# Optimization experiments

Hardware: AMD Instinct MI355X
Metric: run time of the kernel (lower is better)

The kernel has to match this reference:

```python
import jax, jax.numpy as jnp
import numpy as np

N_EMBD = 1024
N_HEAD = 16
HEAD_DIM = N_EMBD // N_HEAD


def setup_inputs() -> dict:
    key = jax.random.key(0)
    k1, k2, k3, k4, k5 = jax.random.split(key, 5)
    B, T, C = 4, 2048, N_EMBD
    s = 1.0 / np.sqrt(C)
    return {
        "x": jax.random.normal(k1, (B, T, C), dtype=jnp.float32),
        "W_attn": jax.random.normal(k2, (C, 3 * C), dtype=jnp.float32) * s,
        "b_attn": jnp.zeros((3 * C,), dtype=jnp.float32),
        "W_proj": jax.random.normal(k3, (C, C), dtype=jnp.float32) * s,
        "b_proj": jnp.zeros((C,), dtype=jnp.float32),
    }


def reference(x, W_attn, b_attn, W_proj, b_proj):
    B, T, C = x.shape
    H, D = N_HEAD, HEAD_DIM
    # fused QKV projection
    qkv = x @ W_attn + b_attn                       # [B,T,3C]
    q, k, v = jnp.split(qkv, 3, axis=2)
    q = q.reshape(B, T, H, D).transpose(0, 2, 1, 3)  # [B,H,T,D]
    k = k.reshape(B, T, H, D).transpose(0, 2, 1, 3)
    v = v.reshape(B, T, H, D).transpose(0, 2, 1, 3)
    # causal scaled dot-product attention
    scale = 1.0 / jnp.sqrt(jnp.asarray(D, dtype=x.dtype))
    scores = jnp.einsum('bhqd,bhkd->bhqk', q, k) * scale  # [B,H,T,T]
    causal = jnp.tril(jnp.ones((T, T), dtype=bool))
    scores = jnp.where(causal[None, None], scores, jnp.finfo(x.dtype).min)
    attn = jax.nn.softmax(scores, axis=-1)
    y = jnp.einsum('bhqk,bhkd->bhqd', attn, v)      # [B,H,T,D]
    y = y.transpose(0, 2, 1, 3).reshape(B, T, C)
    return y @ W_proj + b_proj
```

## Files before the change

kernel.cpp:

```cpp
#include <hip/hip_runtime.h>
#include <hip/hip_bf16.h>
#include <cstdint>

#define B_ 4
#define T_ 2048
#define C_ 1024
#define H_ 16
#define D_ 64
#define M_ (B_*T_)
#define N3 (3*C_)

typedef __bf16 bf16;
typedef __bf16 bf16x8 __attribute__((ext_vector_type(8)));
typedef __bf16 bf16x4 __attribute__((ext_vector_type(4)));
typedef float  floatx4 __attribute__((ext_vector_type(4)));

__device__ __forceinline__ void gl_lds16(const bf16* g, bf16* l) {
  __builtin_amdgcn_global_load_lds(
      (__attribute__((address_space(1))) void*)(void*)g,
      (__attribute__((address_space(3))) void*)(void*)l,
      16, 0, 0);
}

__device__ __forceinline__ uint32_t pack_bf16_trunc(float lo, float hi) {
  union { float f; uint32_t u; } a, b;
  a.f = lo; b.f = hi;
  return (a.u >> 16) | (b.u & 0xffff0000u);
}

__global__ void cast_to_bf16(const float* __restrict__ in, bf16* __restrict__ out, int n) {
  int i = (blockIdx.x * blockDim.x + threadIdx.x) * 4;
  if (i < n) {
    const float4 f = *(const float4*)(in + i);
    bf16x4 o;
    o.x = (bf16)f.x; o.y = (bf16)f.y; o.z = (bf16)f.z; o.w = (bf16)f.w;
    *(bf16x4*)(out + i) = o;
  }
}

__global__ void transpose_cast(const float* __restrict__ in, bf16* __restrict__ out,
                               int R, int C) {
  __shared__ float tile[32][33];
  int r0 = blockIdx.y * 32, c0 = blockIdx.x * 32;
  int tx = threadIdx.x & 31, ty = threadIdx.x >> 5;
  #pragma unroll
  for (int j = 0; j < 32; j += 8)
    tile[ty + j][tx] = in[(size_t)(r0 + ty + j) * C + c0 + tx];
  __syncthreads();
  #pragma unroll
  for (int j = 0; j < 32; j += 8)
    out[(size_t)(c0 + ty + j) * R + r0 + tx] = (bf16)tile[tx][ty + j];
}

__global__ __launch_bounds__(256)
void transpose_v(const bf16* __restrict__ in, bf16* __restrict__ out) {
  __shared__ __attribute__((aligned(16))) bf16 tileN[64 * 64];
  const int tid = threadIdx.x;
  const int bh = blockIdx.z;
  const int t0 = blockIdx.x * 64;
  const int sk = tid >> 2, scc = tid & 3;
  {
    const bf16* p = in + ((size_t)bh * T_ + t0 + sk) * D_ + scc * 16;
    const bf16x8 r0 = *(const bf16x8*)p;
    const bf16x8 r1 = *(const bf16x8*)(p + 8);
    *(bf16x8*)(tileN + sk * 64 + ((2 * scc)     ^ (sk & 7)) * 8) = r0;
    *(bf16x8*)(tileN + sk * 64 + ((2 * scc + 1) ^ (sk & 7)) * 8) = r1;
  }
  __syncthreads();
  const int tc = (tid & 7) * 8;
  #pragma unroll
  for (int half = 0; half < 2; half++) {
    const int d = (tid >> 3) + half * 32;
    bf16x8 o;
    #pragma unroll
    for (int j = 0; j < 8; j++) {
      const int slot = tc + j;
      const int row = (slot & 3) + 4 * ((slot >> 3) & 3) + 16 * ((slot >> 2) & 1)
                    + 32 * (slot >> 5);
      o[j] = tileN[row * 64 + (((d >> 3) ^ (row & 7)) * 8) + (d & 7)];
    }
    *(bf16x8*)(out + ((size_t)bh * D_ + d) * T_ + t0 + tc) = o;
  }
}

template<int MODE>
__global__ __launch_bounds__(256)
void gemm_bt(const bf16* __restrict__ A, const bf16* __restrict__ Bt,
             const float* __restrict__ bias, float* __restrict__ out,
             bf16* __restrict__ qo, bf16* __restrict__ ko, bf16* __restrict__ vo,
             int M, int N, int K)
{
  __shared__ __attribute__((aligned(16))) bf16 As[128 * 32];
  __shared__ __attribute__((aligned(16))) bf16 Bs[128 * 32];

  const int tid  = threadIdx.x;
  const int w    = tid >> 6;
  const int lane = tid & 63;
  const int quad = lane >> 4;
  const int l16  = lane & 15;
  const int wm   = w & 1, wn = w >> 1;
  const int m0   = blockIdx.y * 128, n0 = blockIdx.x * 128;

  floatx4 acc[4][4] = {};

  const int lrow = lane >> 2;
  const int lk   = (lane & 3) * 8;

  const bf16* aptr = A  + (size_t)(m0 + w * 32 + lrow) * K + lk;
  const bf16* bptr = Bt + (size_t)(n0 + w * 32 + lrow) * K + lk;
  bf16* asl = As + w * 1024;
  bf16* bsl = Bs + w * 1024;

  for (int k0 = 0; k0 < K; k0 += 32) {
    gl_lds16(aptr,          asl);
    gl_lds16(aptr + 16 * K, asl + 512);
    gl_lds16(bptr,          bsl);
    gl_lds16(bptr + 16 * K, bsl + 512);
    aptr += 32; bptr += 32;
    __syncthreads();

    bf16x8 af[4], bfb[4];
    #pragma unroll
    for (int i = 0; i < 4; i++)
      af[i] = *(const bf16x8*)(As + (wm * 64 + i * 16 + l16) * 32 + quad * 8);
    #pragma unroll
    for (int i = 0; i < 4; i++)
      bfb[i] = *(const bf16x8*)(Bs + (wn * 64 + i * 16 + l16) * 32 + quad * 8);
    #pragma unroll
    for (int mi = 0; mi < 4; mi++)
      #pragma unroll
      for (int ni = 0; ni < 4; ni++)
        acc[mi][ni] = __builtin_amdgcn_mfma_f32_16x16x32_bf16(af[mi], bfb[ni], acc[mi][ni], 0, 0, 0);
    __syncthreads();
  }

  #pragma unroll
  for (int mi = 0; mi < 4; mi++) {
    #pragma unroll
    for (int ni = 0; ni < 4; ni++) {
      const int col = n0 + wn * 64 + ni * 16 + l16;
      const float bv = bias[col];
      #pragma unroll
      for (int r = 0; r < 4; r++) {
        const int row = m0 + wm * 64 + mi * 16 + quad * 4 + r;
        const float val = acc[mi][ni][r] + bv;
        if (MODE == 0) {
          const int b = row >> 11, t = row & 2047;
          const int s = col >> 10, c = col & 1023;
          const int h = c >> 6,  d = c & 63;
          bf16* dst = (s == 0) ? qo : (s == 1) ? ko : vo;
          dst[((size_t)(b * H_ + h) * T_ + t) * D_ + d] = (bf16)val;
        } else {
          out[(size_t)row * N + col] = val;
        }
      }
    }
  }
}

__device__ __forceinline__ void stage8(const bf16* g, int K, bf16* lds, int lane) {
  const int r = lane >> 3, s = (lane & 7) ^ r;
  gl_lds16(g + (size_t)r * K + s * 8, lds);
}
__device__ __forceinline__ void stage_half(const bf16* g, int K, bf16* lds, int wv, int lane) {
  stage8(g + (size_t)(wv * 16) * K,     K, lds + (wv * 16) * 64, lane);
  stage8(g + (size_t)(wv * 16 + 8) * K, K, lds + (wv * 16 + 8) * 64, lane);
}

#define GBAR  __builtin_amdgcn_s_barrier()
#define WLGKM do { asm volatile("s_waitcnt lgkmcnt(0)"); __builtin_amdgcn_sched_barrier(0); } while (0)
#define WVM4  do { asm volatile("s_waitcnt vmcnt(4)");   __builtin_amdgcn_sched_barrier(0); } while (0)

template<int MODE>
__global__ __launch_bounds__(512, 2)
void gemm256(const bf16* __restrict__ A, const bf16* __restrict__ Bt,
             const float* __restrict__ bias, float* __restrict__ out,
             bf16* __restrict__ qo, bf16* __restrict__ ko, bf16* __restrict__ vo,
             int M, int N, int K)
{
  __shared__ __attribute__((aligned(16))) bf16 As[2][256 * 64];
  __shared__ __attribute__((aligned(16))) bf16 Bs[2][256 * 64];

  const int tid  = threadIdx.x;
  const int wv   = tid >> 6, lane = tid & 63;
  const int quad = lane >> 4, l16 = lane & 15;
  const int wm   = wv >> 2, wn = wv & 3;
  const int NTT  = K >> 6;

  const int nbx = gridDim.x;
  const int nwg = nbx * gridDim.y;
  const int bid = blockIdx.y * nbx + blockIdx.x;
  const int cpx = nwg >> 3;
  const int swz = (bid & 7) * cpx + (bid >> 3);
  const int n0  = (swz % nbx) * 256, m0 = (swz / nbx) * 256;

  floatx4 acc[8][4] = {};

  const bf16* Abase = A  + (size_t)m0 * K;
  const bf16* Bbase = Bt + (size_t)n0 * K;

  stage_half(Abase,                  K, As[0],            wv, lane);
  stage_half(Abase + (size_t)128*K,  K, As[0] + 128 * 64, wv, lane);
  stage_half(Bbase,                  K, Bs[0],            wv, lane);
  stage_half(Bbase + (size_t)128*K,  K, Bs[0] + 128 * 64, wv, lane);
  stage_half(Bbase + 64,             K, Bs[1],            wv, lane);
  stage_half(Abase + 64,             K, As[1],            wv, lane);
  WVM4;
  GBAR;

#define LOADA(qm)                                                          \
  _Pragma("unroll")                                                        \
  for (int mi = 0; mi < 4; mi++) {                                         \
    const int row = wm * 128 + (qm) * 64 + mi * 16 + l16;                  \
    const bf16* rp = bufA + row * 64;                                      \
    af[mi][0] = *(const bf16x8*)(rp + (( quad      ^ (row & 7)) * 8));     \
    af[mi][1] = *(const bf16x8*)(rp + (((4 | quad) ^ (row & 7)) * 8));     \
  }
#define LOADB(qn)                                                          \
  _Pragma("unroll")                                                        \
  for (int ni = 0; ni < 2; ni++) {                                         \
    const int row = wn * 64 + (qn) * 32 + ni * 16 + l16;                   \
    const bf16* rp = bufB + row * 64;                                      \
    bfr[(qn)*2+ni][0] = *(const bf16x8*)(rp + (( quad      ^ (row & 7)) * 8)); \
    bfr[(qn)*2+ni][1] = *(const bf16x8*)(rp + (((4 | quad) ^ (row & 7)) * 8)); \
  }
#define MM(qm, qn)                                                         \
  __builtin_amdgcn_s_setprio(1);                                           \
  _Pragma("unroll")                                                        \
  for (int mi = 0; mi < 4; mi++)                                           \
    _Pragma("unroll")                                                      \
    for (int ni = 0; ni < 2; ni++) {                                       \
      acc[(qm)*4+mi][(qn)*2+ni] = __builtin_amdgcn_mfma_f32_16x16x32_bf16( \
          af[mi][0], bfr[(qn)*2+ni][0], acc[(qm)*4+mi][(qn)*2+ni], 0, 0, 0); \
      acc[(qm)*4+mi][(qn)*2+ni] = __builtin_amdgcn_mfma_f32_16x16x32_bf16( \
          af[mi][1], bfr[(qn)*2+ni][1], acc[(qm)*4+mi][(qn)*2+ni], 0, 0, 0); \
    }                                                                      \
  __builtin_amdgcn_s_setprio(0);

  #pragma unroll 1
  for (int t = 0; t < NTT; t++) {
    const int cur = t & 1;
    const bf16* bufA = As[cur];
    const bf16* bufB = Bs[cur];
    bf16* nA = As[cur ^ 1];
    bf16* nB = Bs[cur ^ 1];
    bf16* cA = As[cur];
    bf16* cB = Bs[cur];
    const int kn1 = (t + 1) * 64, kn2 = (t + 2) * 64;
    const bool h1 = (t + 1 < NTT), h2 = (t + 2 < NTT);

    bf16x8 af[4][2], bfr[4][2];

    LOADA(0);
    LOADB(0);
    if (h1) stage_half(Abase + (size_t)128 * K + kn1, K, nA + 128 * 64, wv, lane);
    GBAR;
    WLGKM;
    MM(0, 0);
    GBAR;

    LOADB(1);
    if (h1) stage_half(Bbase + (size_t)128 * K + kn1, K, nB + 128 * 64, wv, lane);
    GBAR;
    WLGKM;
    MM(0, 1);
    GBAR;

    LOADA(1);
    if (h2) stage_half(Bbase + kn2, K, cB, wv, lane);
    GBAR;
    WLGKM;
    MM(1, 0);
    GBAR;

    if (h2) stage_half(Abase + kn2, K, cA, wv, lane);
    GBAR;
    MM(1, 1);
    WVM4;
    GBAR;
  }

#undef LOADA
#undef LOADB
#undef MM

  #pragma unroll
  for (int mi8 = 0; mi8 < 8; mi8++) {
    #pragma unroll
    for (int nf = 0; nf < 4; nf++) {
      const int col = n0 + wn * 64 + nf * 16 + l16;
      const float bv = bias[col];
      #pragma unroll
      for (int r = 0; r < 4; r++) {
        const int row = m0 + wm * 128 + mi8 * 16 + quad * 4 + r;
        const float val = acc[mi8][nf][r] + bv;
        if (MODE == 0) {
          const int b = row >> 11, tt = row & 2047;
          const int s = col >> 10, c = col & 1023;
          const int h = c >> 6, d = c & 63;
          bf16* dst = (s == 0) ? qo : (s == 1) ? ko : vo;
          dst[((size_t)(b * H_ + h) * T_ + tt) * D_ + d] = (bf16)val;
        } else {
          out[(size_t)row * N + col] = val;
        }
      }
    }
  }
}

__global__ __launch_bounds__(256)
void attn_kernel(const bf16* __restrict__ Q, const bf16* __restrict__ Kp,
                 const bf16* __restrict__ Vtp, bf16* __restrict__ Y)
{
  __shared__ __attribute__((aligned(16))) bf16 Ks[2][64 * 72];
  __shared__ __attribute__((aligned(16))) bf16 Vs[2][64 * 72];

  const int tid  = threadIdx.x;
  const int w    = tid >> 6, lane = tid & 63;
  const int quad = lane >> 4, l16 = lane & 15;
  const int bh = blockIdx.x;
  const int b = bh >> 4, h = bh & 15;

  const int sk = tid >> 2;
  const int sc = (tid & 3) * 16;

  const float SC = 0.125f * 1.44269504088896f;

  const int qt = 15 - (int)blockIdx.y;
  const int q0 = qt * 128;
  const int nch = 2 * qt + 2;

  bf16x8 qf[2][2];
  #pragma unroll
  for (int mt = 0; mt < 2; mt++) {
    const bf16* qp = Q + ((size_t)bh * T_ + q0 + mt * 64 + w * 16 + l16) * D_ + quad * 8;
    qf[mt][0] = *(const bf16x8*)qp;
    qf[mt][1] = *(const bf16x8*)(qp + 32);
  }

  floatx4 o[2][4] = {};
  float l_r[2] = {0.f, 0.f};

  const bf16* kpp = Kp  + (size_t)bh * T_ * D_ + (size_t)sk * D_ + sc;
  const bf16* vpp = Vtp + (size_t)bh * D_ * T_ + (size_t)sk * T_ + sc;

  {
    const bf16x8 k0 = *(const bf16x8*)kpp, k1 = *(const bf16x8*)(kpp + 8);
    const bf16x8 v0 = *(const bf16x8*)vpp, v1 = *(const bf16x8*)(vpp + 8);
    bf16* kd = Ks[0] + sk * 72 + sc;
    *(bf16x8*)kd = k0; *(bf16x8*)(kd + 8) = k1;
    bf16* vd = Vs[0] + sk * 72 + sc;
    *(bf16x8*)vd = v0; *(bf16x8*)(vd + 8) = v1;
    kpp += 64 * D_; vpp += 64;
  }
  __syncthreads();

  #pragma unroll 1
  for (int c = 0; c < nch; c++) {
    const int cur = c & 1;

    bf16x8 nk0, nk1, nv0, nv1;
    const bool have = (c + 1 < nch);
    if (have) {
      nk0 = *(const bf16x8*)kpp; nk1 = *(const bf16x8*)(kpp + 8);
      nv0 = *(const bf16x8*)vpp; nv1 = *(const bf16x8*)(vpp + 8);
      kpp += 64 * D_; vpp += 64;
    }

    const bf16* KsC = Ks[cur];
    const bf16* VsC = Vs[cur];
    const int kv0 = c * 64;
    const bool act0 = (c < nch - 1);

    floatx4 s[2][4];
    #pragma unroll
    for (int nt = 0; nt < 4; nt++) {
      const bf16x8 kf0 = *(const bf16x8*)(KsC + (nt * 16 + l16) * 72 + quad * 8);
      const bf16x8 kf1 = *(const bf16x8*)(KsC + (nt * 16 + l16) * 72 + 32 + quad * 8);
      if (act0) {
        floatx4 z = {};
        z = __builtin_amdgcn_mfma_f32_16x16x32_bf16(kf0, qf[0][0], z, 0, 0, 0);
        s[0][nt] = __builtin_amdgcn_mfma_f32_16x16x32_bf16(kf1, qf[0][1], z, 0, 0, 0);
      }
      floatx4 z = {};
      z = __builtin_amdgcn_mfma_f32_16x16x32_bf16(kf0, qf[1][0], z, 0, 0, 0);
      s[1][nt] = __builtin_amdgcn_mfma_f32_16x16x32_bf16(kf1, qf[1][1], z, 0, 0, 0);
    }

    bf16x8 vfr[4][2];
    #pragma unroll
    for (int nt = 0; nt < 4; nt++) {
      vfr[nt][0] = *(const bf16x8*)(VsC + (nt * 16 + l16) * 72 + quad * 8);
      vfr[nt][1] = *(const bf16x8*)(VsC + (nt * 16 + l16) * 72 + 32 + quad * 8);
    }

    #pragma unroll
    for (int mt = 0; mt < 2; mt++) {
      if (mt == 0 && !act0) continue;
      const bool diag = (c == 2 * qt + mt);
      const int qrow = q0 + mt * 64 + w * 16 + l16;
      float e[4][4];
      float ls0 = 0.f, ls1 = 0.f;
      #pragma unroll
      for (int nt = 0; nt < 4; nt++) {
        #pragma unroll
        for (int r = 0; r < 4; r++) {
          float x = s[mt][nt][r];
          if (diag) {
            if (kv0 + nt * 16 + quad * 4 + r > qrow) x = -1e30f;
          }
          const float ev = __builtin_amdgcn_exp2f(fmaf(x, SC, -8.f));
          e[nt][r] = ev;
          if (nt & 1) ls1 += ev; else ls0 += ev;
        }
      }
      l_r[mt] += ls0 + ls1;

      union { uint32_t u[4]; bf16x8 v; } pa0, pa1;
      #pragma unroll
      for (int jj = 0; jj < 4; jj++) {
        pa0.u[jj] = __builtin_amdgcn_perm(
            __float_as_uint(e[(jj >> 1)][(jj & 1) * 2 + 1]),
            __float_as_uint(e[(jj >> 1)][(jj & 1) * 2]), 0x07060302u);
        pa1.u[jj] = __builtin_amdgcn_perm(
            __float_as_uint(e[2 + (jj >> 1)][(jj & 1) * 2 + 1]),
            __float_as_uint(e[2 + (jj >> 1)][(jj & 1) * 2]), 0x07060302u);
      }
      #pragma unroll
      for (int nt = 0; nt < 4; nt++) {
        o[mt][nt] = __builtin_amdgcn_mfma_f32_16x16x32_bf16(pa0.v, vfr[nt][0], o[mt][nt], 0, 0, 0);
        o[mt][nt] = __builtin_amdgcn_mfma_f32_16x16x32_bf16(pa1.v, vfr[nt][1], o[mt][nt], 0, 0, 0);
      }
    }

    if (have) {
      bf16* kd = Ks[cur ^ 1] + sk * 72 + sc;
      *(bf16x8*)kd = nk0; *(bf16x8*)(kd + 8) = nk1;
      bf16* vd = Vs[cur ^ 1] + sk * 72 + sc;
      *(bf16x8*)vd = nv0; *(bf16x8*)(vd + 8) = nv1;
    }
    __syncthreads();
  }

  #pragma unroll
  for (int mt = 0; mt < 2; mt++) {
    float ls = l_r[mt];
    ls += __shfl_xor(ls, 16);
    ls += __shfl_xor(ls, 32);
    const float invls = 1.f / ls;
    #pragma unroll
    for (int r = 0; r < 4; r++) {
      const float inv = __shfl(invls, (lane & 48) + quad * 4 + r);
      const int t = q0 + mt * 64 + w * 16 + quad * 4 + r;
      #pragma unroll
      for (int nt = 0; nt < 4; nt++)
        Y[((size_t)b * T_ + t) * C_ + h * D_ + nt * 16 + l16] = (bf16)(o[mt][nt][r] * inv);
    }
  }
}

extern "C" void kernel_launch(void* const* d_in, const int* in_sizes, int n_in,
                              void* d_out, int out_size, void* d_ws, size_t ws_size,
                              hipStream_t stream)
{
  const float* x      = (const float*)d_in[0];
  const float* W_attn = (const float*)d_in[1];
  const float* b_attn = (const float*)d_in[2];
  const float* W_proj = (const float*)d_in[3];
  const float* b_proj = (const float*)d_in[4];
  float* out = (float*)d_out;

  bf16* xb  = (bf16*)d_ws;
  bf16* wat = xb  + (size_t)M_ * C_;
  bf16* wpt = wat + (size_t)N3 * C_;
  bf16* qb  = wpt + (size_t)C_ * C_;
  bf16* kb  = qb  + (size_t)M_ * C_;
  bf16* vb  = kb  + (size_t)M_ * C_;
  bf16* yb  = vb  + (size_t)M_ * C_;
  bf16* vtb = xb;

  cast_to_bf16<<<dim3(M_ * C_ / 1024), 256, 0, stream>>>(x, xb, M_ * C_);
  transpose_cast<<<dim3(N3 / 32, C_ / 32), 256, 0, stream>>>(W_attn, wat, C_, N3);
  transpose_cast<<<dim3(C_ / 32, C_ / 32), 256, 0, stream>>>(W_proj, wpt, C_, C_);
  gemm256<0><<<dim3(N3 / 256, M_ / 256), 512, 0, stream>>>(
      xb, wat, b_attn, nullptr, qb, kb, vb, M_, N3, C_);
  transpose_v<<<dim3(T_ / 64, 1, B_ * H_), 256, 0, stream>>>(vb, vtb);
  attn_kernel<<<dim3(B_ * H_, 16), 256, 0, stream>>>(qb, kb, vtb, yb);
  gemm_bt<1><<<dim3(C_ / 128, M_ / 128), 256, 0, stream>>>(
      yb, wpt, b_proj, out, nullptr, nullptr, nullptr, M_, C_, C_);
}
```

Before: 269.3 us.

## Split long causal attention query tiles across two blocks with a combine pass

Query tiles 8-15 are each split into two halves of the KV range, handled by separate blocks that write unnormalized fp32 partial outputs and row sums to workspace. A new combine kernel adds the partials and normalizes into Y, and a lookup table orders the work units for load balancing. The aim is shorter tail latency and better CU occupancy in the causal attention grid. The cost is extra fp32 traffic, one more launch, and reliance on the softmax having no running max, so partials can be summed directly.

Result: slower. 277.3 us (+2.9%).

```diff
diff --git a/kernel.cpp b/kernel.cpp
--- a/kernel.cpp
+++ b/kernel.cpp
@@ -20,12 +20,6 @@
       (__attribute__((address_space(1))) void*)(void*)g,
       (__attribute__((address_space(3))) void*)(void*)l,
       16, 0, 0);
-}
-
-__device__ __forceinline__ uint32_t pack_bf16_trunc(float lo, float hi) {
-  union { float f; uint32_t u; } a, b;
-  a.f = lo; b.f = hi;
-  return (a.u >> 16) | (b.u & 0xffff0000u);
 }
 
 __global__ void cast_to_bf16(const float* __restrict__ in, bf16* __restrict__ out, int n) {
@@ -308,9 +302,14 @@
   }
 }
 
+__device__ const signed char ATT_QT[24]   = {15,15,7,14,14,13,13,6,12,12,11,11,5,10,10,9,9,4,8,8,3,2,1,0};
+__device__ const signed char ATT_PART[24] = { 0, 1,2, 0, 1, 0, 1,2, 0, 1, 0, 1,2, 0, 1,0,1,2,0,1,2,2,2,2};
+
 __global__ __launch_bounds__(256)
 void attn_kernel(const bf16* __restrict__ Q, const bf16* __restrict__ Kp,
-                 const bf16* __restrict__ Vtp, bf16* __restrict__ Y)
+                 const bf16* __restrict__ Vtp, bf16* __restrict__ Y,
+                 float* __restrict__ oa, float* __restrict__ ob,
+                 float* __restrict__ la, float* __restrict__ lb)
 {
   __shared__ __attribute__((aligned(16))) bf16 Ks[2][64 * 72];
   __shared__ __attribute__((aligned(16))) bf16 Vs[2][64 * 72];
@@ -326,9 +325,12 @@
 
   const float SC = 0.125f * 1.44269504088896f;
 
-  const int qt = 15 - (int)blockIdx.y;
+  const int qt   = ATT_QT[blockIdx.y];
+  const int part = ATT_PART[blockIdx.y];
   const int q0 = qt * 128;
   const int nch = 2 * qt + 2;
+  const int c0 = (part == 1) ? qt + 1 : 0;
+  const int c1 = (part == 0) ? qt + 1 : nch;
 
   bf16x8 qf[2][2];
   #pragma unroll
@@ -341,26 +343,26 @@
   floatx4 o[2][4] = {};
   float l_r[2] = {0.f, 0.f};
 
-  const bf16* kpp = Kp  + (size_t)bh * T_ * D_ + (size_t)sk * D_ + sc;
-  const bf16* vpp = Vtp + (size_t)bh * D_ * T_ + (size_t)sk * T_ + sc;
+  const bf16* kpp = Kp  + (size_t)bh * T_ * D_ + (size_t)sk * D_ + sc + (size_t)c0 * 64 * D_;
+  const bf16* vpp = Vtp + (size_t)bh * D_ * T_ + (size_t)sk * T_ + sc + (size_t)c0 * 64;
 
   {
     const bf16x8 k0 = *(const bf16x8*)kpp, k1 = *(const bf16x8*)(kpp + 8);
     const bf16x8 v0 = *(const bf16x8*)vpp, v1 = *(const bf16x8*)(vpp + 8);
-    bf16* kd = Ks[0] + sk * 72 + sc;
+    bf16* kd = Ks[c0 & 1] + sk * 72 + sc;
     *(bf16x8*)kd = k0; *(bf16x8*)(kd + 8) = k1;
-    bf16* vd = Vs[0] + sk * 72 + sc;
+    bf16* vd = Vs[c0 & 1] + sk * 72 + sc;
     *(bf16x8*)vd = v0; *(bf16x8*)(vd + 8) = v1;
     kpp += 64 * D_; vpp += 64;
   }
   __syncthreads();
 
   #pragma unroll 1
-  for (int c = 0; c < nch; c++) {
+  for (int c = c0; c < c1; c++) {
     const int cur = c & 1;
 
     bf16x8 nk0, nk1, nv0, nv1;
-    const bool have = (c + 1 < nch);
+    const bool have = (c + 1 < c1);
     if (have) {
       nk0 = *(const bf16x8*)kpp; nk1 = *(const bf16x8*)(kpp + 8);
       nv0 = *(const bf16x8*)vpp; nv1 = *(const bf16x8*)(vpp + 8);
@@ -442,21 +444,65 @@
     __syncthreads();
   }
 
-  #pragma unroll
-  for (int mt = 0; mt < 2; mt++) {
-    float ls = l_r[mt];
-    ls += __shfl_xor(ls, 16);
-    ls += __shfl_xor(ls, 32);
-    const float invls = 1.f / ls;
-    #pragma unroll
-    for (int r = 0; r < 4; r++) {
-      const float inv = __shfl(invls, (lane & 48) + quad * 4 + r);
-      const int t = q0 + mt * 64 + w * 16 + quad * 4 + r;
-      #pragma unroll
-      for (int nt = 0; nt < 4; nt++)
-        Y[((size_t)b * T_ + t) * C_ + h * D_ + nt * 16 + l16] = (bf16)(o[mt][nt][r] * inv);
-    }
-  }
+  if (part == 2) {
+    #pragma unroll
+    for (int mt = 0; mt < 2; mt++) {
+      float ls = l_r[mt];
+      ls += __shfl_xor(ls, 16);
+      ls += __shfl_xor(ls, 32);
+      const float invls = 1.f / ls;
+      #pragma unroll
+      for (int r = 0; r < 4; r++) {
+        const float inv = __shfl(invls, (lane & 48) + quad * 4 + r);
+        const int t = q0 + mt * 64 + w * 16 + quad * 4 + r;
+        #pragma unroll
+        for (int nt = 0; nt < 4; nt++)
+          Y[((size_t)b * T_ + t) * C_ + h * D_ + nt * 16 + l16] = (bf16)(o[mt][nt][r] * inv);
+      }
+    }
+  } else {
+    float* op = part ? ob : oa;
+    float* lp = part ? lb : la;
+    const int srow = bh * 1024 + (qt - 8) * 128;
+    #pragma unroll
+    for (int mt = 0; mt < 2; mt++) {
+      float ls = l_r[mt];
+      ls += __shfl_xor(ls, 16);
+      ls += __shfl_xor(ls, 32);
+      if (lane < 16)
+        lp[srow + mt * 64 + w * 16 + lane] = ls;
+      #pragma unroll
+      for (int r = 0; r < 4; r++) {
+        const int rr = srow + mt * 64 + w * 16 + quad * 4 + r;
+        #pragma unroll
+        for (int nt = 0; nt < 4; nt++)
+          op[(size_t)rr * 64 + nt * 16 + l16] = o[mt][nt][r];
+      }
+    }
+  }
+}
+
+__global__ __launch_bounds__(256)
+void combine_split(const float* __restrict__ oa, const float* __restrict__ ob,
+                   const float* __restrict__ la, const float* __restrict__ lb,
+                   bf16* __restrict__ Y)
+{
+  const int g = blockIdx.x * 256 + threadIdx.x;
+  const int idx = g * 4;
+  const float4 a = *(const float4*)(oa + idx);
+  const float4 c = *(const float4*)(ob + idx);
+  const int row = idx >> 6;
+  const int d0 = idx & 63;
+  const float inv = 1.f / (la[row] + lb[row]);
+  const int bh = row >> 10, lr = row & 1023;
+  const int bb = bh >> 4, h = bh & 15;
+  bf16* yp = Y + ((size_t)bb * T_ + 1024 + lr) * C_ + h * D_ + d0;
+  bf16x4 ov;
+  ov.x = (bf16)((a.x + c.x) * inv);
+  ov.y = (bf16)((a.y + c.y) * inv);
+  ov.z = (bf16)((a.z + c.z) * inv);
+  ov.w = (bf16)((a.w + c.w) * inv);
+  *(bf16x4*)yp = ov;
 }
 
 extern "C" void kernel_launch(void* const* d_in, const int* in_sizes, int n_in,
@@ -478,6 +524,10 @@
   bf16* vb  = kb  + (size_t)M_ * C_;
   bf16* yb  = vb  + (size_t)M_ * C_;
   bf16* vtb = xb;
+  float* oa = (float*)(yb + (size_t)M_ * C_);
+  float* ob = oa + (size_t)64 * 1024 * 64;
+  float* la = ob + (size_t)64 * 1024 * 64;
+  float* lb = la + (size_t)64 * 1024;
 
   cast_to_bf16<<<dim3(M_ * C_ / 1024), 256, 0, stream>>>(x, xb, M_ * C_);
   transpose_cast<<<dim3(N3 / 32, C_ / 32), 256, 0, stream>>>(W_attn, wat, C_, N3);
@@ -485,7 +535,8 @@
   gemm256<0><<<dim3(N3 / 256, M_ / 256), 512, 0, stream>>>(
       xb, wat, b_attn, nullptr, qb, kb, vb, M_, N3, C_);
   transpose_v<<<dim3(T_ / 64, 1, B_ * H_), 256, 0, stream>>>(vb, vtb);
-  attn_kernel<<<dim3(B_ * H_, 16), 256, 0, stream>>>(qb, kb, vtb, yb);
+  attn_kernel<<<dim3(B_ * H_, 24), 256, 0, stream>>>(qb, kb, vtb, yb, oa, ob, la, lb);
+  combine_split<<<dim3(64 * 1024 * 64 / 1024), 256, 0, stream>>>(oa, ob, la, lb, yb);
   gemm_bt<1><<<dim3(C_ / 128, M_ / 128), 256, 0, stream>>>(
       yb, wpt, b_proj, out, nullptr, nullptr, nullptr, M_, C_, C_);
 }
```

## Load K/V MFMA fragments directly from global memory, dropping LDS staging

Applied to the files above, without the earlier changes.

The attention kernel no longer stages K and V tiles through double-buffered shared memory. Each wave now loads its own MFMA operand fragments straight from global memory every chunk, which removes the LDS writes, the LDS reads and the per-chunk __syncthreads. The cost is that all four waves redundantly fetch the same K/V data through the caches. Loads are also no longer software-prefetched one chunk ahead, so global latency is exposed unless occupancy hides it. The unused pack_bf16_trunc helper is deleted.

New measurement: 328.7 us. 22.0% more time.

```diff
diff --git a/kernel.cpp b/kernel.cpp
--- a/kernel.cpp
+++ b/kernel.cpp
@@ -20,12 +20,6 @@
       (__attribute__((address_space(1))) void*)(void*)g,
       (__attribute__((address_space(3))) void*)(void*)l,
       16, 0, 0);
-}
-
-__device__ __forceinline__ uint32_t pack_bf16_trunc(float lo, float hi) {
-  union { float f; uint32_t u; } a, b;
-  a.f = lo; b.f = hi;
-  return (a.u >> 16) | (b.u & 0xffff0000u);
 }
 
 __global__ void cast_to_bf16(const float* __restrict__ in, bf16* __restrict__ out, int n) {
@@ -312,18 +306,12 @@
 void attn_kernel(const bf16* __restrict__ Q, const bf16* __restrict__ Kp,
                  const bf16* __restrict__ Vtp, bf16* __restrict__ Y)
 {
-  __shared__ __attribute__((aligned(16))) bf16 Ks[2][64 * 72];
-  __shared__ __attribute__((aligned(16))) bf16 Vs[2][64 * 72];
-
   const int tid  = threadIdx.x;
   const int w    = tid >> 6, lane = tid & 63;
   const int quad = lane >> 4, l16 = lane & 15;
   const int bh = blockIdx.x;
   const int b = bh >> 4, h = bh & 15;
 
-  const int sk = tid >> 2;
-  const int sc = (tid & 3) * 16;
-
   const float SC = 0.125f * 1.44269504088896f;
 
   const int qt = 15 - (int)blockIdx.y;
@@ -341,57 +329,42 @@
   floatx4 o[2][4] = {};
   float l_r[2] = {0.f, 0.f};
 
-  const bf16* kpp = Kp  + (size_t)bh * T_ * D_ + (size_t)sk * D_ + sc;
-  const bf16* vpp = Vtp + (size_t)bh * D_ * T_ + (size_t)sk * T_ + sc;
-
-  {
-    const bf16x8 k0 = *(const bf16x8*)kpp, k1 = *(const bf16x8*)(kpp + 8);
-    const bf16x8 v0 = *(const bf16x8*)vpp, v1 = *(const bf16x8*)(vpp + 8);
-    bf16* kd = Ks[0] + sk * 72 + sc;
-    *(bf16x8*)kd = k0; *(bf16x8*)(kd + 8) = k1;
-    bf16* vd = Vs[0] + sk * 72 + sc;
-    *(bf16x8*)vd = v0; *(bf16x8*)(vd + 8) = v1;
-    kpp += 64 * D_; vpp += 64;
-  }
-  __syncthreads();
+  const bf16* kfp = Kp  + ((size_t)bh * T_ + l16) * D_ + quad * 8;
+  const bf16* vfp = Vtp + ((size_t)bh * D_ + l16) * T_ + quad * 8;
 
   #pragma unroll 1
   for (int c = 0; c < nch; c++) {
-    const int cur = c & 1;
-
-    bf16x8 nk0, nk1, nv0, nv1;
-    const bool have = (c + 1 < nch);
-    if (have) {
-      nk0 = *(const bf16x8*)kpp; nk1 = *(const bf16x8*)(kpp + 8);
-      nv0 = *(const bf16x8*)vpp; nv1 = *(const bf16x8*)(vpp + 8);
-      kpp += 64 * D_; vpp += 64;
-    }
-
-    const bf16* KsC = Ks[cur];
-    const bf16* VsC = Vs[cur];
     const int kv0 = c * 64;
     const bool act0 = (c < nch - 1);
 
+    bf16x8 kf[4][2];
+    #pragma unroll
+    for (int nt = 0; nt < 4; nt++) {
+      const bf16* kp = kfp + (size_t)nt * 16 * D_;
+      kf[nt][0] = *(const bf16x8*)kp;
+      kf[nt][1] = *(const bf16x8*)(kp + 32);
+    }
+    bf16x8 vf[4][2];
+    #pragma unroll
+    for (int nt = 0; nt < 4; nt++) {
+      const bf16* vp = vfp + (size_t)nt * 16 * T_;
+      vf[nt][0] = *(const bf16x8*)vp;
+      vf[nt][1] = *(const bf16x8*)(vp + 32);
+    }
+    kfp += 64 * D_;
+    vfp += 64;
+
     floatx4 s[2][4];
     #pragma unroll
     for (int nt = 0; nt < 4; nt++) {
-      const bf16x8 kf0 = *(const bf16x8*)(KsC + (nt * 16 + l16) * 72 + quad * 8);
-      const bf16x8 kf1 = *(const bf16x8*)(KsC + (nt * 16 + l16) * 72 + 32 + quad * 8);
       if (act0) {
         floatx4 z = {};
-        z = __builtin_amdgcn_mfma_f32_16x16x32_bf16(kf0, qf[0][0], z, 0, 0, 0);
-        s[0][nt] = __builtin_amdgcn_mfma_f32_16x16x32_bf16(kf1, qf[0][1], z, 0, 0, 0);
+        z = __builtin_amdgcn_mfma_f32_16x16x32_bf16(kf[nt][0], qf[0][0], z, 0, 0, 0);
+        s[0][nt] = __builtin_amdgcn_mfma_f32_16x16x32_bf16(kf[nt][1], qf[0][1], z, 0, 0, 0);
       }
       floatx4 z = {};
-      z = __builtin_amdgcn_mfma_f32_16x16x32_bf16(kf0, qf[1][0], z, 0, 0, 0);
-      s[1][nt] = __builtin_amdgcn_mfma_f32_16x16x32_bf16(kf1, qf[1][1], z, 0, 0, 0);
-    }
-
-    bf16x8 vfr[4][2];
-    #pragma unroll
-    for (int nt = 0; nt < 4; nt++) {
-      vfr[nt][0] = *(const bf16x8*)(VsC + (nt * 16 + l16) * 72 + quad * 8);
-      vfr[nt][1] = *(const bf16x8*)(VsC + (nt * 16 + l16) * 72 + 32 + quad * 8);
+      z = __builtin_amdgcn_mfma_f32_16x16x32_bf16(kf[nt][0], qf[1][0], z, 0, 0, 0);
+      s[1][nt] = __builtin_amdgcn_mfma_f32_16x16x32_bf16(kf[nt][1], qf[1][1], z, 0, 0, 0);
     }
 
     #pragma unroll
@@ -428,18 +401,10 @@
       }
       #pragma unroll
       for (int nt = 0; nt < 4; nt++) {
-        o[mt][nt] = __builtin_amdgcn_mfma_f32_16x16x32_bf16(pa0.v, vfr[nt][0], o[mt][nt], 0, 0, 0);
-        o[mt][nt] = __builtin_amdgcn_mfma_f32_16x16x32_bf16(pa1.v, vfr[nt][1], o[mt][nt], 0, 0, 0);
-      }
-    }
-
-    if (have) {
-      bf16* kd = Ks[cur ^ 1] + sk * 72 + sc;
-      *(bf16x8*)kd = nk0; *(bf16x8*)(kd + 8) = nk1;
-      bf16* vd = Vs[cur ^ 1] + sk * 72 + sc;
-      *(bf16x8*)vd = nv0; *(bf16x8*)(vd + 8) = nv1;
-    }
-    __syncthreads();
+        o[mt][nt] = __builtin_amdgcn_mfma_f32_16x16x32_bf16(pa0.v, vf[nt][0], o[mt][nt], 0, 0, 0);
+        o[mt][nt] = __builtin_amdgcn_mfma_f32_16x16x32_bf16(pa1.v, vf[nt][1], o[mt][nt], 0, 0, 0);
+      }
+    }
   }
 
   #pragma unroll
```
